# Optimization experiments

Measured on AMD Instinct MI355X. Metric: run time of the kernel, lower is better.

## Reference

```python
import jax, jax.numpy as jnp
import numpy as np

ALPHA = 0.01  # LeakyReLU negative slope


def setup_inputs() -> dict:
    key = jax.random.key(0)
    k1, k2, k3 = jax.random.split(key, 3)
    B, T, F, U, E = 32, 512, 128, 64, 32
    x = jax.random.normal(k1, (B, T, F), dtype=jnp.float32)
    Wg = jax.random.normal(k2, (F, E), dtype=jnp.float32) * (1.0 / np.sqrt(F))
    bg = jnp.zeros((E,), dtype=jnp.float32)
    We = jax.random.normal(k3, (E, F, U), dtype=jnp.float32) * (1.0 / np.sqrt(F))
    be = jnp.zeros((E, U), dtype=jnp.float32)
    return {"x": x, "Wg": Wg, "bg": bg, "We": We, "be": be}


def reference(x, Wg, bg, We, be):
    # gate: linear (no softmax in the original)
    gate = jnp.einsum('btf,fe->bte', x, Wg) + bg            # [B,T,E]
    # all experts as one batched GEMM: [B,T,U,E]
    h = jnp.einsum('btf,efu->btue', x, We) + be.T            # be.T: [U,E]
    h = jnp.where(h >= 0, h, ALPHA * h)                      # LeakyReLU
    # weighted sum over experts
    out = jnp.einsum('btue,bte->btu', h, gate)               # [B,T,U]
    return out
```

## Files before the change

### kernel.cpp

```cpp
#include <hip/hip_runtime.h>
#include <stdint.h>

#define N_TOK 16384
#define F_DIM 128
#define U_DIM 64
#define E_DIM 32
#define MT    64

typedef __bf16 bf16x8 __attribute__((ext_vector_type(8)));
typedef float  floatx4 __attribute__((ext_vector_type(4)));

#define MFMA16(a, b, c) __builtin_amdgcn_mfma_f32_16x16x32_bf16((a), (b), (c), 0, 0, 0)

__device__ __forceinline__ unsigned short f2bf(float f) {
  union { float f; unsigned u; } v; v.f = f;
  unsigned r = v.u + 0x7FFFu + ((v.u >> 16) & 1u);
  return (unsigned short)(r >> 16);
}

__device__ __forceinline__ void async_lds16(const void* g, void* l) {
  __builtin_amdgcn_global_load_lds(
      (const __attribute__((address_space(1))) unsigned int*)g,
      (__attribute__((address_space(3))) unsigned int*)l, 16, 0, 0);
}

__global__ void moe_prep(const float* __restrict__ Wg,
                         const float* __restrict__ We,
                         unsigned short* __restrict__ wsWe,
                         unsigned short* __restrict__ wsWg) {
  int idx = blockIdx.x * 256 + threadIdx.x;
  if (idx < E_DIM * U_DIM * F_DIM) {
    int u = idx & 63;
    int f = (idx >> 6) & 127;
    int e = idx >> 13;
    float v = We[(e << 13) + (f << 6) + u];
    int blk = (f >> 3) ^ (u & 7);
    wsWe[(e << 13) + (u << 7) + (blk << 3) + (f & 7)] = f2bf(v);
  } else {
    int j = idx - E_DIM * U_DIM * F_DIM;
    if (j < E_DIM * F_DIM) {
      int e = j >> 7, f = j & 127;
      wsWg[j] = f2bf(Wg[f * E_DIM + e]);
    }
  }
}

__global__ __launch_bounds__(512, 2) void moe_main(
    const float* __restrict__ x,
    const float* __restrict__ bg,
    const float* __restrict__ be,
    const unsigned short* __restrict__ wsWe,
    const unsigned short* __restrict__ wsWg,
    float* __restrict__ out) {
  __shared__ unsigned short Xs[64 * 136];
  __shared__ unsigned short WeS[2][64 * 128];

  const int tid  = threadIdx.x;
  const int lane = tid & 63;
  const int wid  = tid >> 6;
  const int quad = lane >> 4;
  const int l15  = lane & 15;
  const int mtop = (wid & 1) * 32;
  const int u    = (wid >> 1) * 16 + l15;
  const int base = blockIdx.x * MT;

  {
    const int c0 = wid * 2;
    const unsigned short* g = wsWe + c0 * 512 + lane * 8;
    async_lds16(g, &WeS[0][c0 * 512]);
    async_lds16(g + 512, &WeS[0][(c0 + 1) * 512]);
  }

  {
    const int row = tid >> 3;
    const int c8  = tid & 7;
    const float4* src = (const float4*)(x + (size_t)(base + row) * F_DIM + c8 * 16);
    float4 v0 = src[0], v1 = src[1], v2 = src[2], v3 = src[3];
    union { unsigned short us[16]; uint4 q[2]; } p;
    p.us[0] = f2bf(v0.x); p.us[1] = f2bf(v0.y); p.us[2]  = f2bf(v0.z); p.us[3]  = f2bf(v0.w);
    p.us[4] = f2bf(v1.x); p.us[5] = f2bf(v1.y); p.us[6]  = f2bf(v1.z); p.us[7]  = f2bf(v1.w);
    p.us[8] = f2bf(v2.x); p.us[9] = f2bf(v2.y); p.us[10] = f2bf(v2.z); p.us[11] = f2bf(v2.w);
    p.us[12] = f2bf(v3.x); p.us[13] = f2bf(v3.y); p.us[14] = f2bf(v3.z); p.us[15] = f2bf(v3.w);
    uint4* dst = (uint4*)&Xs[row * 136 + c8 * 16];
    dst[0] = p.q[0];
    dst[1] = p.q[1];
  }
  __syncthreads();

  bf16x8 a[2][4];
#pragma unroll
  for (int mb = 0; mb < 2; mb++)
#pragma unroll
    for (int ks = 0; ks < 4; ks++)
      a[mb][ks] = *(const bf16x8*)&Xs[(mtop + mb * 16 + l15) * 136 + ks * 32 + quad * 8];

  float gate_reg[2][2][4];
#pragma unroll
  for (int mb = 0; mb < 2; mb++) {
#pragma unroll
    for (int et = 0; et < 2; et++) {
      floatx4 g = {0.f, 0.f, 0.f, 0.f};
#pragma unroll
      for (int ks = 0; ks < 4; ks++) {
        bf16x8 wb = *(const bf16x8*)&wsWg[((et << 4) + l15) * 128 + ks * 32 + quad * 8];
        g = MFMA16(a[mb][ks], wb, g);
      }
      float bgv = bg[(et << 4) + l15];
#pragma unroll
      for (int r = 0; r < 4; r++) gate_reg[mb][et][r] = g[r] + bgv;
    }
  }

  float oacc[8];
#pragma unroll
  for (int i = 0; i < 8; i++) oacc[i] = 0.f;

#pragma unroll
  for (int half = 0; half < 2; half++) {
    for (int ee = 0; ee < 16; ee++) {
      const int e = (half << 4) | ee;
      __syncthreads();
      if (e + 1 < E_DIM) {
        const int c0 = wid * 2;
        const unsigned short* g =
            wsWe + (size_t)(e + 1) * 8192 + c0 * 512 + lane * 8;
        async_lds16(g, &WeS[(e + 1) & 1][c0 * 512]);
        async_lds16(g + 512, &WeS[(e + 1) & 1][(c0 + 1) * 512]);
      }
      const float bev = be[e * U_DIM + u];
      const unsigned short* Wb = WeS[e & 1];
      bf16x8 b[4];
#pragma unroll
      for (int ks = 0; ks < 4; ks++) {
        int blk = ((ks << 2) | quad) ^ (u & 7);
        b[ks] = *(const bf16x8*)&Wb[(u << 7) + (blk << 3)];
      }
      floatx4 h0 = {0.f, 0.f, 0.f, 0.f}, h1 = {0.f, 0.f, 0.f, 0.f};
#pragma unroll
      for (int ks = 0; ks < 4; ks++) h0 = MFMA16(a[0][ks], b[ks], h0);
#pragma unroll
      for (int ks = 0; ks < 4; ks++) h1 = MFMA16(a[1][ks], b[ks], h1);

      const int gsrc = (quad << 4) | ee;
#pragma unroll
      for (int r = 0; r < 4; r++) {
        float gv0 = __shfl(gate_reg[0][half][r], gsrc);
        float gv1 = __shfl(gate_reg[1][half][r], gsrc);
        float t0 = h0[r] + bev;
        t0 = fmaxf(t0, 0.f) + 0.01f * fminf(t0, 0.f);
        float t1 = h1[r] + bev;
        t1 = fmaxf(t1, 0.f) + 0.01f * fminf(t1, 0.f);
        oacc[r]     = fmaf(gv0, t0, oacc[r]);
        oacc[4 + r] = fmaf(gv1, t1, oacc[4 + r]);
      }
    }
  }

#pragma unroll
  for (int mb = 0; mb < 2; mb++)
#pragma unroll
    for (int r = 0; r < 4; r++)
      out[(size_t)(base + mtop + mb * 16 + quad * 4 + r) * U_DIM + u] =
          oacc[mb * 4 + r];
}

extern "C" void kernel_launch(void* const* d_in, const int* in_sizes, int n_in,
                              void* d_out, int out_size, void* d_ws, size_t ws_size,
                              hipStream_t stream) {
  const float* x  = (const float*)d_in[0];
  const float* Wg = (const float*)d_in[1];
  const float* bg = (const float*)d_in[2];
  const float* We = (const float*)d_in[3];
  const float* be = (const float*)d_in[4];
  unsigned short* wsWe = (unsigned short*)d_ws;
  unsigned short* wsWg = wsWe + E_DIM * U_DIM * F_DIM;
  (void)in_sizes; (void)n_in; (void)out_size; (void)ws_size;

  moe_prep<<<(E_DIM * U_DIM * F_DIM + E_DIM * F_DIM) / 256, 256, 0, stream>>>(
      Wg, We, wsWe, wsWg);
  moe_main<<<N_TOK / MT, 512, 0, stream>>>(x, bg, be, wsWe, wsWg, (float*)d_out);
}
```

Before: 98.30 us.

## Load expert weights straight to registers in MFMA fragment order, drop LDS pipeline

The prep kernel now packs We and Wg into per-lane MFMA fragment order with 16-byte stores. The main kernel uses 256 threads, with each wave owning 16 output columns across all 64 tokens. Each wave loads B fragments for the next expert directly from global memory into a double-buffered register set, which removes the per-expert LDS staging and __syncthreads barriers. Gate values are staged once in LDS, the bias is folded into the MFMA accumulator init, and LeakyReLU is simplified to one max. The trade-off is higher register pressure and one block per CU, plus L2 traffic from every block reading all the weights.

Measured after the change: 80.76 us. -17.8%, faster.

```diff
diff --git a/kernel.cpp b/kernel.cpp
--- a/kernel.cpp
+++ b/kernel.cpp
@@ -5,7 +5,6 @@
 #define F_DIM 128
 #define U_DIM 64
 #define E_DIM 32
-#define MT    64
 
 typedef __bf16 bf16x8 __attribute__((ext_vector_type(8)));
 typedef float  floatx4 __attribute__((ext_vector_type(4)));
@@ -18,34 +17,30 @@
   return (unsigned short)(r >> 16);
 }
 
-__device__ __forceinline__ void async_lds16(const void* g, void* l) {
-  __builtin_amdgcn_global_load_lds(
-      (const __attribute__((address_space(1))) unsigned int*)g,
-      (__attribute__((address_space(3))) unsigned int*)l, 16, 0, 0);
-}
-
-__global__ void moe_prep(const float* __restrict__ Wg,
-                         const float* __restrict__ We,
-                         unsigned short* __restrict__ wsWe,
-                         unsigned short* __restrict__ wsWg) {
-  int idx = blockIdx.x * 256 + threadIdx.x;
-  if (idx < E_DIM * U_DIM * F_DIM) {
-    int u = idx & 63;
-    int f = (idx >> 6) & 127;
-    int e = idx >> 13;
-    float v = We[(e << 13) + (f << 6) + u];
-    int blk = (f >> 3) ^ (u & 7);
-    wsWe[(e << 13) + (u << 7) + (blk << 3) + (f & 7)] = f2bf(v);
-  } else {
-    int j = idx - E_DIM * U_DIM * F_DIM;
-    if (j < E_DIM * F_DIM) {
-      int e = j >> 7, f = j & 127;
-      wsWg[j] = f2bf(Wg[f * E_DIM + e]);
-    }
+__global__ __launch_bounds__(256) void moe_prep(
+    const float* __restrict__ Wg, const float* __restrict__ We,
+    unsigned short* __restrict__ wsWe, unsigned short* __restrict__ wsWg) {
+  int t = blockIdx.x * 256 + threadIdx.x;
+  if (t < 32768) {
+    int u = t & 63, quad = (t >> 6) & 3, ks = (t >> 8) & 3, e = t >> 10;
+    int f0 = ks * 32 + quad * 8;
+    const float* src = We + e * 8192 + f0 * 64 + u;
+    union { unsigned short us[8]; uint4 q; } p;
+#pragma unroll
+    for (int j = 0; j < 8; j++) p.us[j] = f2bf(src[j * 64]);
+    *(uint4*)(wsWe + t * 8) = p.q;
+  } else if (t < 32768 + 512) {
+    int t2 = t - 32768;
+    int l15 = t2 & 15, quad = (t2 >> 4) & 3, ks = (t2 >> 6) & 3, et = t2 >> 8;
+    int e = et * 16 + l15, f0 = ks * 32 + quad * 8;
+    union { unsigned short us[8]; uint4 q; } p;
+#pragma unroll
+    for (int j = 0; j < 8; j++) p.us[j] = f2bf(Wg[(f0 + j) * 32 + e]);
+    *(uint4*)(wsWg + t2 * 8) = p.q;
   }
 }
 
-__global__ __launch_bounds__(512, 2) void moe_main(
+__global__ __launch_bounds__(256, 1) void moe_main(
     const float* __restrict__ x,
     const float* __restrict__ bg,
     const float* __restrict__ be,
@@ -53,115 +48,118 @@
     const unsigned short* __restrict__ wsWg,
     float* __restrict__ out) {
   __shared__ unsigned short Xs[64 * 136];
-  __shared__ unsigned short WeS[2][64 * 128];
+  __shared__ float Gs[E_DIM][68];
 
   const int tid  = threadIdx.x;
   const int lane = tid & 63;
   const int wid  = tid >> 6;
   const int quad = lane >> 4;
   const int l15  = lane & 15;
-  const int mtop = (wid & 1) * 32;
-  const int u    = (wid >> 1) * 16 + l15;
-  const int base = blockIdx.x * MT;
+  const int u    = wid * 16 + l15;
+  const int base = blockIdx.x * 64;
 
-  {
-    const int c0 = wid * 2;
-    const unsigned short* g = wsWe + c0 * 512 + lane * 8;
-    async_lds16(g, &WeS[0][c0 * 512]);
-    async_lds16(g + 512, &WeS[0][(c0 + 1) * 512]);
-  }
+  bf16x8 bbuf[2][4];
+  float bevb[2];
+#pragma unroll
+  for (int ks = 0; ks < 4; ks++)
+    bbuf[0][ks] = *(const bf16x8*)(wsWe + (size_t)((0 * 4 + ks) * 4 + quad) * 512 + u * 8);
+#pragma unroll
+  for (int ks = 0; ks < 4; ks++)
+    bbuf[1][ks] = *(const bf16x8*)(wsWe + (size_t)((1 * 4 + ks) * 4 + quad) * 512 + u * 8);
+  bevb[0] = be[u];
+  bevb[1] = be[U_DIM + u];
 
-  {
-    const int row = tid >> 3;
-    const int c8  = tid & 7;
-    const float4* src = (const float4*)(x + (size_t)(base + row) * F_DIM + c8 * 16);
+#pragma unroll
+  for (int p = 0; p < 2; p++) {
+    const int row = p * 32 + (tid >> 3);
+    const int c16 = tid & 7;
+    const float4* src = (const float4*)(x + (size_t)(base + row) * F_DIM + c16 * 16);
     float4 v0 = src[0], v1 = src[1], v2 = src[2], v3 = src[3];
-    union { unsigned short us[16]; uint4 q[2]; } p;
-    p.us[0] = f2bf(v0.x); p.us[1] = f2bf(v0.y); p.us[2]  = f2bf(v0.z); p.us[3]  = f2bf(v0.w);
-    p.us[4] = f2bf(v1.x); p.us[5] = f2bf(v1.y); p.us[6]  = f2bf(v1.z); p.us[7]  = f2bf(v1.w);
-    p.us[8] = f2bf(v2.x); p.us[9] = f2bf(v2.y); p.us[10] = f2bf(v2.z); p.us[11] = f2bf(v2.w);
-    p.us[12] = f2bf(v3.x); p.us[13] = f2bf(v3.y); p.us[14] = f2bf(v3.z); p.us[15] = f2bf(v3.w);
-    uint4* dst = (uint4*)&Xs[row * 136 + c8 * 16];
-    dst[0] = p.q[0];
-    dst[1] = p.q[1];
+    union { unsigned short us[16]; uint4 q[2]; } pk;
+    pk.us[0]  = f2bf(v0.x); pk.us[1]  = f2bf(v0.y); pk.us[2]  = f2bf(v0.z); pk.us[3]  = f2bf(v0.w);
+    pk.us[4]  = f2bf(v1.x); pk.us[5]  = f2bf(v1.y); pk.us[6]  = f2bf(v1.z); pk.us[7]  = f2bf(v1.w);
+    pk.us[8]  = f2bf(v2.x); pk.us[9]  = f2bf(v2.y); pk.us[10] = f2bf(v2.z); pk.us[11] = f2bf(v2.w);
+    pk.us[12] = f2bf(v3.x); pk.us[13] = f2bf(v3.y); pk.us[14] = f2bf(v3.z); pk.us[15] = f2bf(v3.w);
+    uint4* dst = (uint4*)&Xs[row * 136 + c16 * 16];
+    dst[0] = pk.q[0];
+    dst[1] = pk.q[1];
   }
   __syncthreads();
 
-  bf16x8 a[2][4];
-#pragma unroll
-  for (int mb = 0; mb < 2; mb++)
+  {
+    bf16x8 ag[4];
 #pragma unroll
     for (int ks = 0; ks < 4; ks++)
-      a[mb][ks] = *(const bf16x8*)&Xs[(mtop + mb * 16 + l15) * 136 + ks * 32 + quad * 8];
-
-  float gate_reg[2][2][4];
-#pragma unroll
-  for (int mb = 0; mb < 2; mb++) {
+      ag[ks] = *(const bf16x8*)&Xs[(wid * 16 + l15) * 136 + ks * 32 + quad * 8];
 #pragma unroll
     for (int et = 0; et < 2; et++) {
       floatx4 g = {0.f, 0.f, 0.f, 0.f};
 #pragma unroll
       for (int ks = 0; ks < 4; ks++) {
-        bf16x8 wb = *(const bf16x8*)&wsWg[((et << 4) + l15) * 128 + ks * 32 + quad * 8];
-        g = MFMA16(a[mb][ks], wb, g);
+        bf16x8 wb = *(const bf16x8*)(wsWg + (size_t)((et * 4 + ks) * 64 + lane) * 8);
+        g = MFMA16(ag[ks], wb, g);
       }
-      float bgv = bg[(et << 4) + l15];
+      float bgv = bg[et * 16 + l15];
 #pragma unroll
-      for (int r = 0; r < 4; r++) gate_reg[mb][et][r] = g[r] + bgv;
+      for (int r = 0; r < 4; r++)
+        Gs[et * 16 + l15][wid * 16 + quad * 4 + r] = g[r] + bgv;
     }
   }
 
-  float oacc[8];
+  bf16x8 a[4][4];
 #pragma unroll
-  for (int i = 0; i < 8; i++) oacc[i] = 0.f;
+  for (int mb = 0; mb < 4; mb++)
+#pragma unroll
+    for (int ks = 0; ks < 4; ks++)
+      a[mb][ks] = *(const bf16x8*)&Xs[(mb * 16 + l15) * 136 + ks * 32 + quad * 8];
+  __syncthreads();
+
+  float oacc[16];
+#pragma unroll
+  for (int i = 0; i < 16; i++) oacc[i] = 0.f;
+
+#pragma unroll 2
+  for (int e = 0; e < E_DIM; ++e) {
+    const int c = e & 1;
+    float g[16];
+#pragma unroll
+    for (int mb = 0; mb < 4; mb++)
+#pragma unroll
+      for (int r = 0; r < 4; r++)
+        g[mb * 4 + r] = Gs[e][mb * 16 + quad * 4 + r];
+
+    const float bev = bevb[c];
+    floatx4 h[4];
+#pragma unroll
+    for (int mb = 0; mb < 4; mb++) h[mb] = {bev, bev, bev, bev};
+#pragma unroll
+    for (int ks = 0; ks < 4; ks++)
+#pragma unroll
+      for (int mb = 0; mb < 4; mb++)
+        h[mb] = MFMA16(a[mb][ks], bbuf[c][ks], h[mb]);
+
+    if (e + 2 < E_DIM) {
+#pragma unroll
+      for (int ks = 0; ks < 4; ks++)
+        bbuf[c][ks] = *(const bf16x8*)(wsWe + (size_t)(((e + 2) * 4 + ks) * 4 + quad) * 512 + u * 8);
+      bevb[c] = be[(e + 2) * U_DIM + u];
+    }
 
 #pragma unroll
-  for (int half = 0; half < 2; half++) {
-    for (int ee = 0; ee < 16; ee++) {
-      const int e = (half << 4) | ee;
-      __syncthreads();
-      if (e + 1 < E_DIM) {
-        const int c0 = wid * 2;
-        const unsigned short* g =
-            wsWe + (size_t)(e + 1) * 8192 + c0 * 512 + lane * 8;
-        async_lds16(g, &WeS[(e + 1) & 1][c0 * 512]);
-        async_lds16(g + 512, &WeS[(e + 1) & 1][(c0 + 1) * 512]);
-      }
-      const float bev = be[e * U_DIM + u];
-      const unsigned short* Wb = WeS[e & 1];
-      bf16x8 b[4];
-#pragma unroll
-      for (int ks = 0; ks < 4; ks++) {
-        int blk = ((ks << 2) | quad) ^ (u & 7);
-        b[ks] = *(const bf16x8*)&Wb[(u << 7) + (blk << 3)];
-      }
-      floatx4 h0 = {0.f, 0.f, 0.f, 0.f}, h1 = {0.f, 0.f, 0.f, 0.f};
-#pragma unroll
-      for (int ks = 0; ks < 4; ks++) h0 = MFMA16(a[0][ks], b[ks], h0);
-#pragma unroll
-      for (int ks = 0; ks < 4; ks++) h1 = MFMA16(a[1][ks], b[ks], h1);
-
-      const int gsrc = (quad << 4) | ee;
+    for (int mb = 0; mb < 4; mb++)
 #pragma unroll
       for (int r = 0; r < 4; r++) {
-        float gv0 = __shfl(gate_reg[0][half][r], gsrc);
-        float gv1 = __shfl(gate_reg[1][half][r], gsrc);
-        float t0 = h0[r] + bev;
-        t0 = fmaxf(t0, 0.f) + 0.01f * fminf(t0, 0.f);
-        float t1 = h1[r] + bev;
-        t1 = fmaxf(t1, 0.f) + 0.01f * fminf(t1, 0.f);
-        oacc[r]     = fmaf(gv0, t0, oacc[r]);
-        oacc[4 + r] = fmaf(gv1, t1, oacc[4 + r]);
+        float t = h[mb][r];
+        t = fmaxf(t, 0.01f * t);
+        oacc[mb * 4 + r] = fmaf(g[mb * 4 + r], t, oacc[mb * 4 + r]);
       }
-    }
   }
 
 #pragma unroll
-  for (int mb = 0; mb < 2; mb++)
+  for (int mb = 0; mb < 4; mb++)
 #pragma unroll
     for (int r = 0; r < 4; r++)
-      out[(size_t)(base + mtop + mb * 16 + quad * 4 + r) * U_DIM + u] =
-          oacc[mb * 4 + r];
+      out[(size_t)(base + mb * 16 + quad * 4 + r) * U_DIM + u] = oacc[mb * 4 + r];
 }
 
 extern "C" void kernel_launch(void* const* d_in, const int* in_sizes, int n_in,
@@ -176,7 +174,6 @@
   unsigned short* wsWg = wsWe + E_DIM * U_DIM * F_DIM;
   (void)in_sizes; (void)n_in; (void)out_size; (void)ws_size;
 
-  moe_prep<<<(E_DIM * U_DIM * F_DIM + E_DIM * F_DIM) / 256, 256, 0, stream>>>(
-      Wg, We, wsWe, wsWg);
-  moe_main<<<N_TOK / MT, 512, 0, stream>>>(x, bg, be, wsWe, wsWg, (float*)d_out);
+  moe_prep<<<130, 256, 0, stream>>>(Wg, We, wsWe, wsWg);
+  moe_main<<<N_TOK / 64, 256, 0, stream>>>(x, bg, be, wsWe, wsWg, (float*)d_out);
 }
```
